# Kernel tuning notes

Hardware: AMD Instinct MI355X
Metric: run time of the kernel (lower is better)

## Reference

```python
import jax, jax.numpy as jnp
import numpy as np

D_MODEL = 1024
NUM_HEADS = 16
D_FF = 4096
EPS = 1e-5


def _linear(x, w, b):
    # torch nn.Linear: y = x @ W^T + b, W is [out, in]
    return jnp.einsum('bld,od->blo', x, w) + b


def _layer_norm(x, g, b):
    mu = jnp.mean(x, axis=-1, keepdims=True)
    var = jnp.mean(jnp.square(x - mu), axis=-1, keepdims=True)
    return (x - mu) / jnp.sqrt(var + EPS) * g + b


def _mha(q, k, v, wq, bq, wk, bk, wv, bv, wo, bo, mask, num_heads):
    B, Lq, D = q.shape
    hd = D // num_heads
    Q = _linear(q, wq, bq).reshape(B, Lq, num_heads, hd).transpose(0, 2, 1, 3)
    K = _linear(k, wk, bk).reshape(B, -1, num_heads, hd).transpose(0, 2, 1, 3)
    V = _linear(v, wv, bv).reshape(B, -1, num_heads, hd).transpose(0, 2, 1, 3)
    scale = jnp.sqrt(jnp.asarray(hd, dtype=q.dtype))
    energy = jnp.einsum('bhqd,bhkd->bhqk', Q, K) / scale  # [B,H,Lq,Lk]
    energy = jnp.where(mask, energy, jnp.asarray(-1e10, dtype=q.dtype))
    attn = jax.nn.softmax(energy, axis=-1)
    x = jnp.einsum('bhqk,bhkd->bhqd', attn, V)
    x = x.transpose(0, 2, 1, 3).reshape(B, Lq, D)
    return _linear(x, wo, bo), attn


def setup_inputs() -> dict:
    key = jax.random.key(0)
    ks = iter(jax.random.split(key, 40))
    B, T, S, D, F = 4, 1024, 1024, D_MODEL, D_FF
    inp = {
        'tgt': jax.random.normal(next(ks), (B, T, D), dtype=jnp.float32),
        'enc_src': jax.random.normal(next(ks), (B, S, D), dtype=jnp.float32),
        'tgt_mask': jnp.tril(jnp.ones((1, 1, T, T), dtype=bool)),
        'src_mask': jnp.ones((1, 1, 1, S), dtype=bool),
    }
    def lin(kk, o, i):
        return jax.random.normal(kk, (o, i), dtype=jnp.float32) * 0.02
    for pfx in ('sa', 'ca'):  # self-attn and cross-attn params
        for nm in ('q', 'k', 'v', 'o'):
            inp[f'{pfx}_w{nm}'] = lin(next(ks), D, D)
            inp[f'{pfx}_b{nm}'] = jnp.zeros((D,), dtype=jnp.float32)
    inp['ff_w1'] = lin(next(ks), F, D)
    inp['ff_b1'] = jnp.zeros((F,), dtype=jnp.float32)
    inp['ff_w2'] = lin(next(ks), D, F)
    inp['ff_b2'] = jnp.zeros((D,), dtype=jnp.float32)
    for i in (1, 2, 3):
        inp[f'ln{i}_g'] = jnp.ones((D,), dtype=jnp.float32)
        inp[f'ln{i}_b'] = jnp.zeros((D,), dtype=jnp.float32)
    return inp


def reference(tgt, enc_src, tgt_mask, src_mask,
              sa_wq, sa_bq, sa_wk, sa_bk, sa_wv, sa_bv, sa_wo, sa_bo,
              ca_wq, ca_bq, ca_wk, ca_bk, ca_wv, ca_bv, ca_wo, ca_bo,
              ff_w1, ff_b1, ff_w2, ff_b2,
              ln1_g, ln1_b, ln2_g, ln2_b, ln3_g, ln3_b):
    # dropout in eval mode (identity)
    _t, _ = _mha(tgt, tgt, tgt, sa_wq, sa_bq, sa_wk, sa_bk, sa_wv, sa_bv,
                 sa_wo, sa_bo, tgt_mask, NUM_HEADS)
    tgt = _layer_norm(tgt + _t, ln1_g, ln1_b)
    _t, attention = _mha(tgt, enc_src, enc_src, ca_wq, ca_bq, ca_wk, ca_bk,
                         ca_wv, ca_bv, ca_wo, ca_bo, src_mask, NUM_HEADS)
    tgt = _layer_norm(tgt + _t, ln2_g, ln2_b)
    _t = _linear(jax.nn.relu(_linear(tgt, ff_w1, ff_b1)), ff_w2, ff_b2)
    tgt = _layer_norm(tgt + _t, ln3_g, ln3_b)
    return tgt, attention
```

## Files before the change

kernel.cpp:

```cpp
#include <hip/hip_runtime.h>
#include <hip/hip_bf16.h>

#define BBATCH 4
#define TT 1024
#define SS 1024
#define DD 1024
#define HH 16
#define HD 64
#define FFD 4096
#define MM (BBATCH*TT)

using f32x4  = __attribute__((ext_vector_type(4))) float;
using s16x8  = __attribute__((ext_vector_type(8))) short;
using bf16x8 = __attribute__((ext_vector_type(8))) __bf16;

__device__ __forceinline__ unsigned short f2b(float f) {
  union { float f; unsigned int u; } x{f};
  unsigned int r = x.u + 0x7FFFu + ((x.u >> 16) & 1u);
  return (unsigned short)(r >> 16);
}

__device__ __forceinline__ float b2f(unsigned short u) {
  union { unsigned int i; float f; } x; x.i = (unsigned int)u << 16; return x.f;
}

__device__ __forceinline__ void gload16(const void* g, void* l) {
  __builtin_amdgcn_global_load_lds(
      (const __attribute__((address_space(1))) void*)g,
      (__attribute__((address_space(3))) void*)l, 16, 0, 0);
}

__device__ __forceinline__ f32x4 mfma_bf16(s16x8 a, s16x8 b, f32x4 c) {
  return __builtin_amdgcn_mfma_f32_16x16x32_bf16(
      __builtin_bit_cast(bf16x8, a), __builtin_bit_cast(bf16x8, b), c, 0, 0, 0);
}

__device__ __forceinline__ void xcd_swz(int gx, int& bn, int& bm) {
  int flat = blockIdx.y * gx + blockIdx.x;
  int nwg = gx * gridDim.y;
  int swz = (flat & 7) * (nwg >> 3) + (flat >> 3);
  bn = swz % gx; bm = swz / gx;
}

template <int JT, int NSUB>
__device__ __forceinline__ void gemm_core(
    const unsigned short* __restrict__ Ab, int lda,
    const unsigned short* __restrict__ Bb, int ldb,
    int K, unsigned short* As, unsigned short* Bs, f32x4 (&acc)[4][JT])
{
  const int tid = threadIdx.x, wave = tid >> 6, lane = tid & 63;
  const int r0 = tid >> 2, c0 = (tid & 3) * 8;
  const int wrow = (wave >> 1) * 64, wcol = (wave & 1) * 16 * JT;
  const int q = lane >> 4, rl = lane & 15;
  const s16x8* Av = (const s16x8*)As;
  const s16x8* Bv = (const s16x8*)Bs;

  for (int k0 = 0; k0 < K; k0 += 32 * NSUB) {
#pragma unroll
    for (int s = 0; s < NSUB; s++) {
      int kk = k0 + s * 32;
      gload16(Ab + (size_t)r0 * lda + kk + c0, As + s * 4096 + wave * 512);
      gload16(Ab + (size_t)(r0 + 64) * lda + kk + c0, As + s * 4096 + wave * 512 + 2048);
      gload16(Bb + (size_t)r0 * ldb + kk + c0, Bs + s * (JT * 1024) + wave * 512);
      if (JT == 4)
        gload16(Bb + (size_t)(r0 + 64) * ldb + kk + c0, Bs + s * (JT * 1024) + wave * 512 + 2048);
    }
    __syncthreads();
#pragma unroll
    for (int s = 0; s < NSUB; s++) {
      s16x8 af[4], bfr[JT];
#pragma unroll
      for (int t = 0; t < 4; t++) af[t] = Av[s * 512 + (wrow + t * 16 + rl) * 4 + q];
#pragma unroll
      for (int t = 0; t < JT; t++) bfr[t] = Bv[s * (JT * 128) + (wcol + t * 16 + rl) * 4 + q];
#pragma unroll
      for (int i = 0; i < 4; i++)
#pragma unroll
        for (int j = 0; j < JT; j++)
          acc[i][j] = mfma_bf16(af[i], bfr[j], acc[i][j]);
    }
    __syncthreads();
  }
}

template <int EPI, int JT, int NSUB>
__global__ __launch_bounds__(256) void gemm_bt(
    const unsigned short* __restrict__ A, int lda,
    const unsigned short* __restrict__ B, int ldb,
    const float* __restrict__ bias, const float* __restrict__ res,
    float* __restrict__ Cf, unsigned short* __restrict__ Cb, int ldc, int K)
{
  __shared__ __align__(16) unsigned short As[NSUB * 128 * 32];
  __shared__ __align__(16) unsigned short Bs[NSUB * JT * 1024];
  int bm, bn;
  xcd_swz(gridDim.x, bn, bm);
  const int lane = threadIdx.x & 63, wave = threadIdx.x >> 6;
  const int wrow = (wave >> 1) * 64, wcol = (wave & 1) * 16 * JT;
  const int q = lane >> 4, rl = lane & 15;

  f32x4 acc[4][JT];
  f32x4 z = {0.f, 0.f, 0.f, 0.f};
#pragma unroll
  for (int i = 0; i < 4; i++)
#pragma unroll
    for (int j = 0; j < JT; j++) acc[i][j] = z;

  gemm_core<JT, NSUB>(A + (size_t)bm * 128 * lda, lda,
                      B + (size_t)bn * (32 * JT) * ldb, ldb, K, As, Bs, acc);

#pragma unroll
  for (int i = 0; i < 4; i++) {
    int gm0 = bm * 128 + wrow + i * 16 + q * 4;
#pragma unroll
    for (int j = 0; j < JT; j++) {
      int gn = bn * (32 * JT) + wcol + j * 16 + rl;
      float bv = bias[gn];
#pragma unroll
      for (int r = 0; r < 4; r++) {
        size_t off = (size_t)(gm0 + r) * ldc + gn;
        float v = acc[i][j][r];
        if constexpr (EPI == 0) Cb[off] = f2b(v + bv);
        else if constexpr (EPI == 2) Cf[off] = v + bv + res[off];
        else Cb[off] = f2b(fmaxf(v + bv, 0.f));
      }
    }
  }
}

__global__ __launch_bounds__(256) void gemm_qkvkv(
    const unsigned short* __restrict__ Xb, const unsigned short* __restrict__ Eb,
    const unsigned short* __restrict__ Wqkv1, const unsigned short* __restrict__ Wkv2,
    const float* __restrict__ bqkv, const float* __restrict__ bkv,
    unsigned short* __restrict__ QKVb, unsigned short* __restrict__ KVb,
    unsigned short* __restrict__ Vt1, unsigned short* __restrict__ Vt2)
{
  __shared__ __align__(16) unsigned short lds[16384];
  unsigned short* As = lds;
  unsigned short* Bs = lds + 8192;
  const int tid = threadIdx.x;
  int bm, bn;
  xcd_swz(gridDim.x, bn, bm);
  const int lane = tid & 63, wave = tid >> 6;
  const int wrow = (wave >> 1) * 64, wcol = (wave & 1) * 64;
  const int q = lane >> 4, rl = lane & 15;

  const unsigned short *A, *Bw;
  const float* bias;
  unsigned short *C, *Vt;
  int ldc, vbn;
  bool isV;
  if (bn < 24) {
    A = Xb; Bw = Wqkv1 + (size_t)bn * 128 * 1024; bias = bqkv + bn * 128;
    C = QKVb + bn * 128; ldc = 3072;
    isV = (bn >= 16); Vt = Vt1; vbn = bn - 16;
  } else {
    int b2 = bn - 24;
    A = Eb; Bw = Wkv2 + (size_t)b2 * 128 * 1024; bias = bkv + b2 * 128;
    C = KVb + b2 * 128; ldc = 2048;
    isV = (b2 >= 8); Vt = Vt2; vbn = b2 - 8;
  }

  f32x4 acc[4][4];
  f32x4 z = {0.f, 0.f, 0.f, 0.f};
#pragma unroll
  for (int i = 0; i < 4; i++)
#pragma unroll
    for (int j = 0; j < 4; j++) acc[i][j] = z;

  gemm_core<4, 2>(A + (size_t)bm * 128 * 1024, 1024, Bw, 1024, 1024, As, Bs, acc);

  if (!isV) {
#pragma unroll
    for (int i = 0; i < 4; i++) {
      int lr0 = wrow + i * 16 + q * 4;
#pragma unroll
      for (int j = 0; j < 4; j++) {
        int lc = wcol + j * 16 + rl;
        float bv = bias[lc];
#pragma unroll
        for (int r = 0; r < 4; r++)
          C[(size_t)(bm * 128 + lr0 + r) * ldc + lc] = f2b(acc[i][j][r] + bv);
      }
    }
  } else {
#pragma unroll
    for (int i = 0; i < 4; i++) {
      int lr0 = wrow + i * 16 + q * 4;
#pragma unroll
      for (int j = 0; j < 4; j++) {
        int lc = wcol + j * 16 + rl;
        float bv = bias[lc];
        int base = lc * 128, sw = (lc & 7) << 2;
#pragma unroll
        for (int r = 0; r < 4; r++)
          lds[base + ((lr0 + r) ^ sw)] = f2b(acc[i][j][r] + bv);
      }
    }
    __syncthreads();
    const int b = bm >> 3, s0 = (bm & 7) * 128;
#pragma unroll
    for (int it = 0; it < 16; it++) {
      int idx = it * 256 + tid;
      int lc = idx >> 5, qa = idx & 31;
      ushort4 v4 = *(const ushort4*)&lds[lc * 128 + ((qa ^ (lc & 7)) << 2)];
      int h = vbn * 2 + (lc >> 6), d = lc & 63;
      *(ushort4*)&Vt[(((size_t)b * 16 + h) * 64 + d) * 1024 + s0 + qa * 4] = v4;
    }
  }
}

__device__ __forceinline__ void stage_k(
    const unsigned short* src, int ldk, unsigned short* Kbuf,
    int r0, int c0, int wave)
{
#pragma unroll
  for (int kq = 0; kq < 2; kq++) {
    gload16(src + (size_t)r0 * ldk + kq * 32 + c0, Kbuf + kq * 4096 + wave * 512);
    gload16(src + (size_t)(r0 + 64) * ldk + kq * 32 + c0, Kbuf + kq * 4096 + wave * 512 + 2048);
  }
}

__device__ __forceinline__ void sblock_qk(
    const unsigned short* Qs, const unsigned short* Ks,
    int wrow, int wcol, int q, int rl, f32x4 (&acc)[4][4])
{
  const s16x8* Qv = (const s16x8*)Qs;
  const s16x8* Kv = (const s16x8*)Ks;
  f32x4 z = {0.f, 0.f, 0.f, 0.f};
#pragma unroll
  for (int i = 0; i < 4; i++)
#pragma unroll
    for (int j = 0; j < 4; j++) acc[i][j] = z;
#pragma unroll
  for (int kq = 0; kq < 2; kq++) {
    s16x8 af[4], bf[4];
#pragma unroll
    for (int t = 0; t < 4; t++) af[t] = Qv[kq * 512 + (wrow + t * 16 + rl) * 4 + q];
#pragma unroll
    for (int t = 0; t < 4; t++) bf[t] = Kv[kq * 512 + (wcol + t * 16 + rl) * 4 + q];
#pragma unroll
    for (int i = 0; i < 4; i++)
#pragma unroll
      for (int j = 0; j < 4; j++)
        acc[i][j] = mfma_bf16(af[i], bf[j], acc[i][j]);
  }
}

__device__ __forceinline__ void load_vf(
    const unsigned short* Vbase, int c, int wc2, int q, int rl, s16x8 (&vf)[4][2])
{
#pragma unroll
  for (int ks = 0; ks < 4; ks++)
#pragma unroll
    for (int t = 0; t < 2; t++)
      vf[ks][t] = *(const s16x8*)(Vbase + (size_t)(wc2 + t * 16 + rl) * SS +
                                  c * 128 + ks * 32 + q * 8);
}

__device__ __forceinline__ void store_ps_swz(
    unsigned short* Ps, const f32x4 (&acc)[4][4], int wrow, int wcol, int q, int rl)
{
#pragma unroll
  for (int i = 0; i < 4; i++)
#pragma unroll
    for (int j = 0; j < 4; j++) {
      int col = wcol + j * 16 + rl;
      int ks = col >> 5, cc = col & 31;
#pragma unroll
      for (int r = 0; r < 4; r++) {
        int row = wrow + i * 16 + q * 4 + r;
        int unit = (row * 4 + (cc >> 3)) ^ ((row >> 1) & 3);
        Ps[ks * 4096 + unit * 8 + (cc & 7)] = f2b(acc[i][j][r]);
      }
    }
}

__device__ __forceinline__ void pv_swz(
    const unsigned short* Ps, const s16x8 (&vf)[4][2],
    int wrow, int q, int rl, f32x4 (&oacc)[4][2])
{
  const s16x8* Pv = (const s16x8*)Ps;
#pragma unroll
  for (int ks = 0; ks < 4; ks++) {
    s16x8 af[4];
#pragma unroll
    for (int t = 0; t < 4; t++) {
      int row = wrow + t * 16 + rl;
      af[t] = Pv[ks * 512 + ((row * 4 + q) ^ ((row >> 1) & 3))];
    }
#pragma unroll
    for (int i = 0; i < 4; i++)
#pragma unroll
      for (int jt = 0; jt < 2; jt++)
        oacc[i][jt] = mfma_bf16(af[i], vf[ks][jt], oacc[i][jt]);
  }
}

__global__ __launch_bounds__(256, 2) void flash_sa(
    const unsigned short* __restrict__ Qg, int ldq,
    const unsigned short* __restrict__ Kg, int ldk,
    const unsigned short* __restrict__ Vt,
    unsigned short* __restrict__ Og)
{
  __shared__ __align__(16) unsigned short Qs[2 * 128 * 32];
  __shared__ __align__(16) unsigned short Ks[2][2 * 128 * 32];
  __shared__ __align__(16) unsigned short Ps[4 * 128 * 32];

  const int tid = threadIdx.x, wave = tid >> 6, lane = tid & 63;
  const int q = lane >> 4, rl = lane & 15;
  const int bh = blockIdx.y, b = bh >> 4, h = bh & 15;
  const int bm = (bh & 32) ? (7 - blockIdx.x) : blockIdx.x;
  const int wrow = (wave >> 1) * 64, wcol = (wave & 1) * 64;
  const int wc2 = (wave & 1) * 32;
  const int r0 = tid >> 2, c0 = (tid & 3) * 8;

  const unsigned short* Qbase = Qg + ((size_t)b * TT + bm * 128) * ldq + h * HD;
  const unsigned short* Kbase = Kg + (size_t)b * SS * ldk + h * HD;
  const unsigned short* Vbase = Vt + ((size_t)bh << 16);

#pragma unroll
  for (int kq = 0; kq < 2; kq++) {
    gload16(Qbase + (size_t)r0 * ldq + kq * 32 + c0, Qs + kq * 4096 + wave * 512);
    gload16(Qbase + (size_t)(r0 + 64) * ldq + kq * 32 + c0, Qs + kq * 4096 + wave * 512 + 2048);
  }
  stage_k(Kbase, ldk, Ks[0], r0, c0, wave);
  const int nch = bm + 1;

  float l_run[4][4];
  f32x4 oacc[4][2];
  f32x4 z = {0.f, 0.f, 0.f, 0.f};
#pragma unroll
  for (int i = 0; i < 4; i++) {
    oacc[i][0] = z; oacc[i][1] = z;
#pragma unroll
    for (int r = 0; r < 4; r++) l_run[i][r] = 0.f;
  }

  for (int c = 0; c < nch; c++) {
    __syncthreads();
    if (c + 1 < nch)
      stage_k(Kbase + (size_t)(c + 1) * 128 * ldk, ldk, Ks[(c + 1) & 1], r0, c0, wave);
    s16x8 vf[4][2];
    load_vf(Vbase, c, wc2, q, rl, vf);
    f32x4 acc[4][4];
    sblock_qk(Qs, Ks[c & 1], wrow, wcol, q, rl, acc);
#pragma unroll
    for (int i = 0; i < 4; i++)
#pragma unroll
      for (int r = 0; r < 4; r++) {
#pragma unroll
        for (int j = 0; j < 4; j++) {
          float v = acc[i][j][r] * 0.125f;
          bool msk = (c == bm) && (wcol + j * 16 + rl) > (wrow + i * 16 + q * 4 + r);
          acc[i][j][r] = msk ? 0.f : __expf(v);
        }
        float s = acc[i][0][r] + acc[i][1][r] + acc[i][2][r] + acc[i][3][r];
#pragma unroll
        for (int off = 1; off < 16; off <<= 1) s += __shfl_xor(s, off);
        l_run[i][r] += s;
      }
    store_ps_swz(Ps, acc, wrow, wcol, q, rl);
    __syncthreads();
    pv_swz(Ps, vf, wrow, q, rl, oacc);
  }
  __syncthreads();

  float* red = (float*)Ps;
  if (rl == 0) {
#pragma unroll
    for (int i = 0; i < 4; i++)
#pragma unroll
      for (int r = 0; r < 4; r++)
        red[(wave & 1) * 128 + wrow + i * 16 + q * 4 + r] = l_run[i][r];
  }
  __syncthreads();

#pragma unroll
  for (int i = 0; i < 4; i++) {
#pragma unroll
    for (int r = 0; r < 4; r++) {
      int row = wrow + i * 16 + q * 4 + r;
      float inv = 1.0f / (red[row] + red[128 + row]);
      int grow = bm * 128 + row;
#pragma unroll
      for (int jt = 0; jt < 2; jt++) {
        int col = h * HD + wc2 + jt * 16 + rl;
        Og[((size_t)b * TT + grow) * DD + col] = f2b(oacc[i][jt][r] * inv);
      }
    }
  }
}

__global__ __launch_bounds__(256, 2) void flash_ca(
    const unsigned short* __restrict__ Qg, int ldq,
    const unsigned short* __restrict__ Kg, int ldk,
    const unsigned short* __restrict__ Vt,
    float* __restrict__ Pout,
    unsigned short* __restrict__ Og)
{
  __shared__ __align__(16) unsigned short Qs[2 * 128 * 32];
  __shared__ __align__(16) unsigned short Ks[2][2 * 128 * 32];
  __shared__ __align__(16) unsigned short Ps[4 * 128 * 32];

  const int tid = threadIdx.x, wave = tid >> 6, lane = tid & 63;
  const int q = lane >> 4, rl = lane & 15;
  const int bm = blockIdx.x, bh = blockIdx.y, b = bh >> 4, h = bh & 15;
  const int wrow = (wave >> 1) * 64, wcol = (wave & 1) * 64;
  const int wc2 = (wave & 1) * 32;
  const int r0 = tid >> 2, c0 = (tid & 3) * 8;

  const unsigned short* Qbase = Qg + ((size_t)b * TT + bm * 128) * ldq + h * HD;
  const unsigned short* Kbase = Kg + (size_t)b * SS * ldk + h * HD;
  const unsigned short* Vbase = Vt + ((size_t)bh << 16);

#pragma unroll
  for (int kq = 0; kq < 2; kq++) {
    gload16(Qbase + (size_t)r0 * ldq + kq * 32 + c0, Qs + kq * 4096 + wave * 512);
    gload16(Qbase + (size_t)(r0 + 64) * ldq + kq * 32 + c0, Qs + kq * 4096 + wave * 512 + 2048);
  }
  stage_k(Kbase, ldk, Ks[0], r0, c0, wave);

  float l_run[4][4];
#pragma unroll
  for (int i = 0; i < 4; i++)
#pragma unroll
    for (int r = 0; r < 4; r++) l_run[i][r] = 0.f;

  for (int c = 0; c < 8; c++) {
    __syncthreads();
    if (c < 7)
      stage_k(Kbase + (size_t)(c + 1) * 128 * ldk, ldk, Ks[(c + 1) & 1], r0, c0, wave);
    f32x4 acc[4][4];
    sblock_qk(Qs, Ks[c & 1], wrow, wcol, q, rl, acc);
#pragma unroll
    for (int i = 0; i < 4; i++)
#pragma unroll
      for (int r = 0; r < 4; r++) {
        float s = __expf(acc[i][0][r] * 0.125f) + __expf(acc[i][1][r] * 0.125f) +
                  __expf(acc[i][2][r] * 0.125f) + __expf(acc[i][3][r] * 0.125f);
#pragma unroll
        for (int off = 1; off < 16; off <<= 1) s += __shfl_xor(s, off);
        l_run[i][r] += s;
      }
  }
  float* red = (float*)Ps;
  if (rl == 0) {
#pragma unroll
    for (int i = 0; i < 4; i++)
#pragma unroll
      for (int r = 0; r < 4; r++)
        red[(wave & 1) * 128 + wrow + i * 16 + q * 4 + r] = l_run[i][r];
  }
  __syncthreads();
  float invl[4][4];
#pragma unroll
  for (int i = 0; i < 4; i++)
#pragma unroll
    for (int r = 0; r < 4; r++) {
      int row = wrow + i * 16 + q * 4 + r;
      invl[i][r] = 1.0f / (red[row] + red[128 + row]);
    }

  f32x4 oacc[4][2];
  f32x4 z = {0.f, 0.f, 0.f, 0.f};
#pragma unroll
  for (int i = 0; i < 4; i++) { oacc[i][0] = z; oacc[i][1] = z; }
  stage_k(Kbase, ldk, Ks[0], r0, c0, wave);

  for (int c = 0; c < 8; c++) {
    __syncthreads();
    if (c < 7)
      stage_k(Kbase + (size_t)(c + 1) * 128 * ldk, ldk, Ks[(c + 1) & 1], r0, c0, wave);
    s16x8 vf[4][2];
    load_vf(Vbase, c, wc2, q, rl, vf);
    f32x4 acc[4][4];
    sblock_qk(Qs, Ks[c & 1], wrow, wcol, q, rl, acc);
#pragma unroll
    for (int i = 0; i < 4; i++)
#pragma unroll
      for (int j = 0; j < 4; j++)
#pragma unroll
        for (int r = 0; r < 4; r++)
          acc[i][j][r] = __expf(acc[i][j][r] * 0.125f) * invl[i][r];
    store_ps_swz(Ps, acc, wrow, wcol, q, rl);
    __syncthreads();
#pragma unroll
    for (int it = 0; it < 8; it++) {
      int idx = it * 256 + tid;
      int ks = idx >> 9, rw = (idx >> 2) & 127, u = idx & 3;
      s16x8 pv = ((const s16x8*)Ps)[ks * 512 + ((rw * 4 + u) ^ ((rw >> 1) & 3))];
      float4 lo = make_float4(b2f((unsigned short)pv[0]), b2f((unsigned short)pv[1]),
                              b2f((unsigned short)pv[2]), b2f((unsigned short)pv[3]));
      float4 hi = make_float4(b2f((unsigned short)pv[4]), b2f((unsigned short)pv[5]),
                              b2f((unsigned short)pv[6]), b2f((unsigned short)pv[7]));
      float* dst = Pout + ((size_t)bh << 20) + ((size_t)(bm * 128 + rw) << 10) +
                   c * 128 + ks * 32 + u * 8;
      ((float4*)dst)[0] = lo;
      ((float4*)dst)[1] = hi;
    }
    pv_swz(Ps, vf, wrow, q, rl, oacc);
  }

#pragma unroll
  for (int i = 0; i < 4; i++)
#pragma unroll
    for (int jt = 0; jt < 2; jt++)
#pragma unroll
      for (int r = 0; r < 4; r++) {
        int row = bm * 128 + wrow + i * 16 + q * 4 + r;
        int col = h * HD + wc2 + jt * 16 + rl;
        Og[((size_t)b * TT + row) * DD + col] = f2b(oacc[i][jt][r]);
      }
}

__global__ __launch_bounds__(256) void ln_k(
    const float* __restrict__ src, const float* __restrict__ g,
    const float* __restrict__ b, float* __restrict__ dstf,
    unsigned short* __restrict__ dstb)
{
  __shared__ float sh[10];
  const size_t row = blockIdx.x;
  const int tid = threadIdx.x;
  float4 v = ((const float4*)(src + (row << 10)))[tid];
  float s = v.x + v.y + v.z + v.w;
  float ss = v.x * v.x + v.y * v.y + v.z * v.z + v.w * v.w;
  for (int o = 32; o; o >>= 1) { s += __shfl_down(s, o); ss += __shfl_down(ss, o); }
  if ((tid & 63) == 0) { sh[tid >> 6] = s; sh[4 + (tid >> 6)] = ss; }
  __syncthreads();
  if (tid == 0) {
    sh[8] = sh[0] + sh[1] + sh[2] + sh[3];
    sh[9] = sh[4] + sh[5] + sh[6] + sh[7];
  }
  __syncthreads();
  const float mean = sh[8] * (1.0f / DD);
  const float var = sh[9] * (1.0f / DD) - mean * mean;
  const float inv = rsqrtf(var + 1e-5f);
  float4 gv = ((const float4*)g)[tid];
  float4 bv = ((const float4*)b)[tid];
  float4 y;
  y.x = (v.x - mean) * inv * gv.x + bv.x;
  y.y = (v.y - mean) * inv * gv.y + bv.y;
  y.z = (v.z - mean) * inv * gv.z + bv.z;
  y.w = (v.w - mean) * inv * gv.w + bv.w;
  if (dstf) ((float4*)(dstf + (row << 10)))[tid] = y;
  if (dstb) {
    ushort4 o = make_ushort4(f2b(y.x), f2b(y.y), f2b(y.z), f2b(y.w));
    ((ushort4*)(dstb + (row << 10)))[tid] = o;
  }
}

struct CvtArgs {
  const float* src[12];
  unsigned short* dst[12];
};

__global__ __launch_bounds__(256) void cvt_all(CvtArgs a) {
  constexpr int st[13] = {0,       1048576, 2097152, 2359296, 2621440,
                          2883584, 3145728, 3407872, 3670016, 3932160,
                          4194304, 5242880, 6291456};
  int i = blockIdx.x * 256 + threadIdx.x;
  int s = 0;
#pragma unroll
  for (int k = 1; k < 12; k++) s += (i >= st[k]) ? 1 : 0;
  int j = i - st[s];
  float4 v = ((const float4*)a.src[s])[j];
  ushort4 o = make_ushort4(f2b(v.x), f2b(v.y), f2b(v.z), f2b(v.w));
  ((ushort4*)a.dst[s])[j] = o;
}

__global__ __launch_bounds__(256) void bias_pack(
    const float* __restrict__ bq, const float* __restrict__ bk, const float* __restrict__ bv,
    const float* __restrict__ bk2, const float* __restrict__ bv2,
    float* __restrict__ bqkv, float* __restrict__ bkv)
{
  int i = blockIdx.x * 256 + threadIdx.x;
  if (i < 1024) bqkv[i] = bq[i];
  else if (i < 2048) bqkv[i] = bk[i - 1024];
  else if (i < 3072) bqkv[i] = bv[i - 2048];
  else if (i < 4096) bkv[i - 3072] = bk2[i - 3072];
  else if (i < 5120) bkv[i - 3072] = bv2[i - 4096 + 1024];
}


extern "C" void kernel_launch(void* const* d_in, const int* in_sizes, int n_in,
                              void* d_out, int out_size, void* d_ws, size_t ws_size,
                              hipStream_t stream)
{
  const float* tgt = (const float*)d_in[0];
  const float* enc = (const float*)d_in[1];
  const float* sa_wq = (const float*)d_in[4];  const float* sa_bq = (const float*)d_in[5];
  const float* sa_wk = (const float*)d_in[6];  const float* sa_bk = (const float*)d_in[7];
  const float* sa_wv = (const float*)d_in[8];  const float* sa_bv = (const float*)d_in[9];
  const float* sa_wo = (const float*)d_in[10]; const float* sa_bo = (const float*)d_in[11];
  const float* ca_wq = (const float*)d_in[12]; const float* ca_bq = (const float*)d_in[13];
  const float* ca_wk = (const float*)d_in[14]; const float* ca_bk = (const float*)d_in[15];
  const float* ca_wv = (const float*)d_in[16]; const float* ca_bv = (const float*)d_in[17];
  const float* ca_wo = (const float*)d_in[18]; const float* ca_bo = (const float*)d_in[19];
  const float* ff_w1 = (const float*)d_in[20]; const float* ff_b1 = (const float*)d_in[21];
  const float* ff_w2 = (const float*)d_in[22]; const float* ff_b2 = (const float*)d_in[23];
  const float* ln1_g = (const float*)d_in[24]; const float* ln1_b = (const float*)d_in[25];
  const float* ln2_g = (const float*)d_in[26]; const float* ln2_b = (const float*)d_in[27];
  const float* ln3_g = (const float*)d_in[28]; const float* ln3_b = (const float*)d_in[29];

  float* out_tgt = (float*)d_out;
  float* out_attn = (float*)d_out + (size_t)MM * DD;

  char* w = (char*)d_ws;
  size_t off = 0;
  auto alloc = [&](size_t bytes) { void* p = w + off; off += (bytes + 255) & ~(size_t)255; return p; };
  unsigned short* Xb   = (unsigned short*)alloc((size_t)MM * DD * 2);
  unsigned short* Eb   = (unsigned short*)alloc((size_t)MM * DD * 2);
  unsigned short* Wq1  = (unsigned short*)alloc((size_t)DD * DD * 2);
  unsigned short* Wk1  = (unsigned short*)alloc((size_t)DD * DD * 2);
  unsigned short* Wv1  = (unsigned short*)alloc((size_t)DD * DD * 2);
  unsigned short* Wo1  = (unsigned short*)alloc((size_t)DD * DD * 2);
  unsigned short* Wq2  = (unsigned short*)alloc((size_t)DD * DD * 2);
  unsigned short* Wk2  = (unsigned short*)alloc((size_t)DD * DD * 2);
  unsigned short* Wv2  = (unsigned short*)alloc((size_t)DD * DD * 2);
  unsigned short* Wo2  = (unsigned short*)alloc((size_t)DD * DD * 2);
  unsigned short* Wf1  = (unsigned short*)alloc((size_t)FFD * DD * 2);
  unsigned short* Wf2  = (unsigned short*)alloc((size_t)DD * FFD * 2);
  unsigned short* QKVb = (unsigned short*)alloc((size_t)MM * 3 * DD * 2);
  unsigned short* KVb  = (unsigned short*)alloc((size_t)MM * 2 * DD * 2);
  unsigned short* Qca  = (unsigned short*)alloc((size_t)MM * DD * 2);
  unsigned short* Vt1  = (unsigned short*)alloc((size_t)MM * DD * 2);
  unsigned short* Vt2  = (unsigned short*)alloc((size_t)MM * DD * 2);
  unsigned short* Ob   = (unsigned short*)alloc((size_t)MM * DD * 2);
  float*          res1 = (float*)alloc((size_t)MM * DD * 4);
  unsigned short* t1b  = (unsigned short*)alloc((size_t)MM * DD * 2);
  float*          res2 = (float*)alloc((size_t)MM * DD * 4);
  unsigned short* t2b  = (unsigned short*)alloc((size_t)MM * DD * 2);
  unsigned short* Fb   = (unsigned short*)alloc((size_t)MM * FFD * 2);
  float*          bqkv = (float*)alloc(3072 * 4);
  float*          bkv  = (float*)alloc(2048 * 4);

  CvtArgs ca;
  ca.src[0] = tgt;   ca.dst[0] = Xb;
  ca.src[1] = enc;   ca.dst[1] = Eb;
  ca.src[2] = sa_wq; ca.dst[2] = Wq1;
  ca.src[3] = sa_wk; ca.dst[3] = Wk1;
  ca.src[4] = sa_wv; ca.dst[4] = Wv1;
  ca.src[5] = sa_wo; ca.dst[5] = Wo1;
  ca.src[6] = ca_wq; ca.dst[6] = Wq2;
  ca.src[7] = ca_wk; ca.dst[7] = Wk2;
  ca.src[8] = ca_wv; ca.dst[8] = Wv2;
  ca.src[9] = ca_wo; ca.dst[9] = Wo2;
  ca.src[10] = ff_w1; ca.dst[10] = Wf1;
  ca.src[11] = ff_w2; ca.dst[11] = Wf2;

  bias_pack<<<20, 256, 0, stream>>>(sa_bq, sa_bk, sa_bv, ca_bk, ca_bv, bqkv, bkv);
  cvt_all<<<24576, 256, 0, stream>>>(ca);

  const dim3 gPRJ(40, 32);
  const dim3 gN64(16, 32);
  const dim3 gFF1(32, 32);
  const dim3 gFl(8, 64);

  gemm_qkvkv<<<gPRJ, 256, 0, stream>>>(Xb, Eb, Wq1, Wk2, bqkv, bkv,
                                       QKVb, KVb, Vt1, Vt2);

  flash_sa<<<gFl, 256, 0, stream>>>(QKVb, 3 * DD, QKVb + DD, 3 * DD, Vt1, Ob);
  gemm_bt<2, 2, 4><<<gN64, 256, 0, stream>>>(Ob, DD, Wo1, DD, sa_bo, tgt, res1, nullptr, DD, DD);
  ln_k<<<MM, 256, 0, stream>>>(res1, ln1_g, ln1_b, res1, t1b);

  gemm_bt<0, 2, 4><<<gN64, 256, 0, stream>>>(t1b, DD, Wq2, DD, ca_bq, nullptr, nullptr, Qca, DD, DD);
  flash_ca<<<gFl, 256, 0, stream>>>(Qca, DD, KVb, 2 * DD, Vt2, out_attn, Ob);
  gemm_bt<2, 2, 4><<<gN64, 256, 0, stream>>>(Ob, DD, Wo2, DD, ca_bo, res1, res2, nullptr, DD, DD);
  ln_k<<<MM, 256, 0, stream>>>(res2, ln2_g, ln2_b, res2, t2b);

  gemm_bt<3, 4, 2><<<gFF1, 256, 0, stream>>>(t2b, DD, Wf1, DD, ff_b1, nullptr, nullptr, Fb, FFD, DD);
  gemm_bt<2, 2, 4><<<gN64, 256, 0, stream>>>(Fb, FFD, Wf2, FFD, ff_b2, res2, res1, nullptr, DD, FFD);
  ln_k<<<MM, 256, 0, stream>>>(res1, ln3_g, ln3_b, out_tgt, nullptr);
}
```

Measured before the change: 768.8 us.

## Double-buffer LDS in GEMM core and fold bias packing into conversion kernel

Replaces the single-buffered GEMM main loop with a double-buffered one. Asynchronous global-to-LDS loads for the next 64-wide K tile are issued before computing the current tile, so only one barrier per iteration is needed. This aims to hide global load latency behind MFMA work, at the cost of doubled LDS usage, which may lower occupancy. It also merges the separate bias_pack kernel into cvt_all as extra blocks, removing one launch.

```diff
diff --git a/kernel.cpp b/kernel.cpp
--- a/kernel.cpp
+++ b/kernel.cpp
@@ -42,8 +42,25 @@
   bn = swz % gx; bm = swz / gx;
 }
 
-template <int JT, int NSUB>
-__device__ __forceinline__ void gemm_core(
+template <int JT>
+__device__ __forceinline__ void stage_ab(
+    const unsigned short* __restrict__ Ab, int lda,
+    const unsigned short* __restrict__ Bb, int ldb,
+    int kk, unsigned short* As, unsigned short* Bs, int r0, int c0, int wave)
+{
+#pragma unroll
+  for (int s = 0; s < 2; s++) {
+    int k2 = kk + s * 32;
+    gload16(Ab + (size_t)r0 * lda + k2 + c0, As + s * 4096 + wave * 512);
+    gload16(Ab + (size_t)(r0 + 64) * lda + k2 + c0, As + s * 4096 + wave * 512 + 2048);
+    gload16(Bb + (size_t)r0 * ldb + k2 + c0, Bs + s * (JT * 1024) + wave * 512);
+    if (JT == 4)
+      gload16(Bb + (size_t)(r0 + 64) * ldb + k2 + c0, Bs + s * (JT * 1024) + wave * 512 + 2048);
+  }
+}
+
+template <int JT>
+__device__ __forceinline__ void gemm_core_db(
     const unsigned short* __restrict__ Ab, int lda,
     const unsigned short* __restrict__ Bb, int ldb,
     int K, unsigned short* As, unsigned short* Bs, f32x4 (&acc)[4][JT])
@@ -52,46 +69,42 @@
   const int r0 = tid >> 2, c0 = (tid & 3) * 8;
   const int wrow = (wave >> 1) * 64, wcol = (wave & 1) * 16 * JT;
   const int q = lane >> 4, rl = lane & 15;
-  const s16x8* Av = (const s16x8*)As;
-  const s16x8* Bv = (const s16x8*)Bs;
-
-  for (int k0 = 0; k0 < K; k0 += 32 * NSUB) {
-#pragma unroll
-    for (int s = 0; s < NSUB; s++) {
-      int kk = k0 + s * 32;
-      gload16(Ab + (size_t)r0 * lda + kk + c0, As + s * 4096 + wave * 512);
-      gload16(Ab + (size_t)(r0 + 64) * lda + kk + c0, As + s * 4096 + wave * 512 + 2048);
-      gload16(Bb + (size_t)r0 * ldb + kk + c0, Bs + s * (JT * 1024) + wave * 512);
-      if (JT == 4)
-        gload16(Bb + (size_t)(r0 + 64) * ldb + kk + c0, Bs + s * (JT * 1024) + wave * 512 + 2048);
-    }
-    __syncthreads();
-#pragma unroll
-    for (int s = 0; s < NSUB; s++) {
+
+  stage_ab<JT>(Ab, lda, Bb, ldb, 0, As, Bs, r0, c0, wave);
+  const int nt = K >> 6;
+  for (int t = 0; t < nt; t++) {
+    __syncthreads();
+    if (t + 1 < nt)
+      stage_ab<JT>(Ab, lda, Bb, ldb, (t + 1) << 6,
+                   As + ((t + 1) & 1) * 8192, Bs + ((t + 1) & 1) * (JT * 2048),
+                   r0, c0, wave);
+    const s16x8* Av = (const s16x8*)(As + (t & 1) * 8192);
+    const s16x8* Bv = (const s16x8*)(Bs + (t & 1) * (JT * 2048));
+#pragma unroll
+    for (int s = 0; s < 2; s++) {
       s16x8 af[4], bfr[JT];
 #pragma unroll
-      for (int t = 0; t < 4; t++) af[t] = Av[s * 512 + (wrow + t * 16 + rl) * 4 + q];
-#pragma unroll
-      for (int t = 0; t < JT; t++) bfr[t] = Bv[s * (JT * 128) + (wcol + t * 16 + rl) * 4 + q];
+      for (int u = 0; u < 4; u++) af[u] = Av[s * 512 + (wrow + u * 16 + rl) * 4 + q];
+#pragma unroll
+      for (int u = 0; u < JT; u++) bfr[u] = Bv[s * (JT * 128) + (wcol + u * 16 + rl) * 4 + q];
 #pragma unroll
       for (int i = 0; i < 4; i++)
 #pragma unroll
         for (int j = 0; j < JT; j++)
           acc[i][j] = mfma_bf16(af[i], bfr[j], acc[i][j]);
     }
-    __syncthreads();
-  }
-}
-
-template <int EPI, int JT, int NSUB>
+  }
+}
+
+template <int EPI, int JT>
 __global__ __launch_bounds__(256) void gemm_bt(
     const unsigned short* __restrict__ A, int lda,
     const unsigned short* __restrict__ B, int ldb,
     const float* __restrict__ bias, const float* __restrict__ res,
     float* __restrict__ Cf, unsigned short* __restrict__ Cb, int ldc, int K)
 {
-  __shared__ __align__(16) unsigned short As[NSUB * 128 * 32];
-  __shared__ __align__(16) unsigned short Bs[NSUB * JT * 1024];
+  __shared__ __align__(16) unsigned short As[2 * 8192];
+  __shared__ __align__(16) unsigned short Bs[2 * JT * 2048];
   int bm, bn;
   xcd_swz(gridDim.x, bn, bm);
   const int lane = threadIdx.x & 63, wave = threadIdx.x >> 6;
@@ -105,8 +118,8 @@
 #pragma unroll
     for (int j = 0; j < JT; j++) acc[i][j] = z;
 
-  gemm_core<JT, NSUB>(A + (size_t)bm * 128 * lda, lda,
-                      B + (size_t)bn * (32 * JT) * ldb, ldb, K, As, Bs, acc);
+  gemm_core_db<JT>(A + (size_t)bm * 128 * lda, lda,
+                   B + (size_t)bn * (32 * JT) * ldb, ldb, K, As, Bs, acc);
 
 #pragma unroll
   for (int i = 0; i < 4; i++) {
@@ -134,9 +147,9 @@
     unsigned short* __restrict__ QKVb, unsigned short* __restrict__ KVb,
     unsigned short* __restrict__ Vt1, unsigned short* __restrict__ Vt2)
 {
-  __shared__ __align__(16) unsigned short lds[16384];
+  __shared__ __align__(16) unsigned short lds[32768];
   unsigned short* As = lds;
-  unsigned short* Bs = lds + 8192;
+  unsigned short* Bs = lds + 16384;
   const int tid = threadIdx.x;
   int bm, bn;
   xcd_swz(gridDim.x, bn, bm);
@@ -167,7 +180,7 @@
 #pragma unroll
     for (int j = 0; j < 4; j++) acc[i][j] = z;
 
-  gemm_core<4, 2>(A + (size_t)bm * 128 * 1024, 1024, Bw, 1024, 1024, As, Bs, acc);
+  gemm_core_db<4>(A + (size_t)bm * 128 * 1024, 1024, Bw, 1024, 1024, As, Bs, acc);
 
   if (!isV) {
 #pragma unroll
@@ -183,6 +196,7 @@
       }
     }
   } else {
+    __syncthreads();
 #pragma unroll
     for (int i = 0; i < 4; i++) {
       int lr0 = wrow + i * 16 + q * 4;
@@ -552,13 +566,25 @@
 struct CvtArgs {
   const float* src[12];
   unsigned short* dst[12];
+  const float *bq, *bk, *bv, *bk2, *bv2;
+  float *bqkv, *bkv;
 };
 
 __global__ __launch_bounds__(256) void cvt_all(CvtArgs a) {
+  const int blk = blockIdx.x;
+  if (blk >= 24576) {
+    int i = (blk - 24576) * 256 + threadIdx.x;
+    if (i < 1024) a.bqkv[i] = a.bq[i];
+    else if (i < 2048) a.bqkv[i] = a.bk[i - 1024];
+    else if (i < 3072) a.bqkv[i] = a.bv[i - 2048];
+    else if (i < 4096) a.bkv[i - 3072] = a.bk2[i - 3072];
+    else if (i < 5120) a.bkv[i - 3072] = a.bv2[i - 4096 + 1024];
+    return;
+  }
   constexpr int st[13] = {0,       1048576, 2097152, 2359296, 2621440,
                           2883584, 3145728, 3407872, 3670016, 3932160,
                           4194304, 5242880, 6291456};
-  int i = blockIdx.x * 256 + threadIdx.x;
+  int i = blk * 256 + threadIdx.x;
   int s = 0;
 #pragma unroll
   for (int k = 1; k < 12; k++) s += (i >= st[k]) ? 1 : 0;
@@ -566,19 +592,6 @@
   float4 v = ((const float4*)a.src[s])[j];
   ushort4 o = make_ushort4(f2b(v.x), f2b(v.y), f2b(v.z), f2b(v.w));
   ((ushort4*)a.dst[s])[j] = o;
-}
-
-__global__ __launch_bounds__(256) void bias_pack(
-    const float* __restrict__ bq, const float* __restrict__ bk, const float* __restrict__ bv,
-    const float* __restrict__ bk2, const float* __restrict__ bv2,
-    float* __restrict__ bqkv, float* __restrict__ bkv)
-{
-  int i = blockIdx.x * 256 + threadIdx.x;
-  if (i < 1024) bqkv[i] = bq[i];
-  else if (i < 2048) bqkv[i] = bk[i - 1024];
-  else if (i < 3072) bqkv[i] = bv[i - 2048];
-  else if (i < 4096) bkv[i - 3072] = bk2[i - 3072];
-  else if (i < 5120) bkv[i - 3072] = bv2[i - 4096 + 1024];
 }
 
 
@@ -647,9 +660,10 @@
   ca.src[9] = ca_wo; ca.dst[9] = Wo2;
   ca.src[10] = ff_w1; ca.dst[10] = Wf1;
   ca.src[11] = ff_w2; ca.dst[11] = Wf2;
-
-  bias_pack<<<20, 256, 0, stream>>>(sa_bq, sa_bk, sa_bv, ca_bk, ca_bv, bqkv, bkv);
-  cvt_all<<<24576, 256, 0, stream>>>(ca);
+  ca.bq = sa_bq; ca.bk = sa_bk; ca.bv = sa_bv; ca.bk2 = ca_bk; ca.bv2 = ca_bv;
+  ca.bqkv = bqkv; ca.bkv = bkv;
+
+  cvt_all<<<24596, 256, 0, stream>>>(ca);
 
   const dim3 gPRJ(40, 32);
   const dim3 gN64(16, 32);
@@ -660,15 +674,15 @@
                                        QKVb, KVb, Vt1, Vt2);
 
   flash_sa<<<gFl, 256, 0, stream>>>(QKVb, 3 * DD, QKVb + DD, 3 * DD, Vt1, Ob);
-  gemm_bt<2, 2, 4><<<gN64, 256, 0, stream>>>(Ob, DD, Wo1, DD, sa_bo, tgt, res1, nullptr, DD, DD);
+  gemm_bt<2, 2><<<gN64, 256, 0, stream>>>(Ob, DD, Wo1, DD, sa_bo, tgt, res1, nullptr, DD, DD);
   ln_k<<<MM, 256, 0, stream>>>(res1, ln1_g, ln1_b, res1, t1b);
 
-  gemm_bt<0, 2, 4><<<gN64, 256, 0, stream>>>(t1b, DD, Wq2, DD, ca_bq, nullptr, nullptr, Qca, DD, DD);
+  gemm_bt<0, 2><<<gN64, 256, 0, stream>>>(t1b, DD, Wq2, DD, ca_bq, nullptr, nullptr, Qca, DD, DD);
   flash_ca<<<gFl, 256, 0, stream>>>(Qca, DD, KVb, 2 * DD, Vt2, out_attn, Ob);
-  gemm_bt<2, 2, 4><<<gN64, 256, 0, stream>>>(Ob, DD, Wo2, DD, ca_bo, res1, res2, nullptr, DD, DD);
+  gemm_bt<2, 2><<<gN64, 256, 0, stream>>>(Ob, DD, Wo2, DD, ca_bo, res1, res2, nullptr, DD, DD);
   ln_k<<<MM, 256, 0, stream>>>(res2, ln2_g, ln2_b, res2, t2b);
 
-  gemm_bt<3, 4, 2><<<gFF1, 256, 0, stream>>>(t2b, DD, Wf1, DD, ff_b1, nullptr, nullptr, Fb, FFD, DD);
-  gemm_bt<2, 2, 4><<<gN64, 256, 0, stream>>>(Fb, FFD, Wf2, FFD, ff_b2, res2, res1, nullptr, DD, FFD);
+  gemm_bt<3, 4><<<gFF1, 256, 0, stream>>>(t2b, DD, Wf1, DD, ff_b1, nullptr, nullptr, Fb, FFD, DD);
+  gemm_bt<2, 2><<<gN64, 256, 0, stream>>>(Fb, FFD, Wf2, FFD, ff_b2, res2, res1, nullptr, DD, FFD);
   ln_k<<<MM, 256, 0, stream>>>(res1, ln3_g, ln3_b, out_tgt, nullptr);
 }
```

Measured after the change: 762.6 us (median of 3 runs). No clear change (-0.8%).
